# Optimization experiments

Measured on AMD Instinct MI355X. Metric: run time of the kernel, lower is better.

## Reference

```python
import jax, jax.numpy as jnp
import numpy as np

B, T, DIM = 1, 4096, 768
H, D = 6, 128  # num_heads, head_dim
ATTN_SCALE = 0.12
EPS = 1.1920929e-07  # torch fp32 rms_norm default eps


def _rms_norm(x):
    # F.rms_norm over last dim, no learned weight
    return x * jax.lax.rsqrt(jnp.mean(jnp.square(x), axis=-1, keepdims=True) + EPS)


def _rotary_tables(seq_len, head_dim):
    # angular_freq: (1/1024)**linspace(0,1,D//4) concat zeros(D//4) -> length D//2
    af = (1.0 / 1024.0) ** jnp.linspace(0.0, 1.0, head_dim // 4, dtype=jnp.float32)
    af = jnp.concatenate([af, jnp.zeros(head_dim // 4, dtype=jnp.float32)])
    t = jnp.arange(seq_len, dtype=jnp.float32)
    theta = t[:, None] * af[None, :]  # [T, D//2]
    return jnp.cos(theta), jnp.sin(theta)


def _apply_rotary(x_bthd, cos, sin):
    # x: [B,T,H,D]; rotate pairs (x1, x2) = halves of last dim
    x1, x2 = jnp.split(x_bthd.astype(jnp.float32), 2, axis=-1)
    c = cos[None, :, None, :]
    s = sin[None, :, None, :]
    y1 = x1 * c + x2 * s
    y2 = -x1 * s + x2 * c
    return jnp.concatenate([y1, y2], axis=-1).astype(x_bthd.dtype)


def setup_inputs() -> dict:
    key = jax.random.key(0)
    k1, k2, k3, k4, k5 = jax.random.split(key, 5)
    std = 0.5 * DIM ** (-0.5)
    bound = (3.0 ** 0.5) * std
    x = jax.random.normal(k1, (B, T, DIM), dtype=jnp.float32)
    ve = jax.random.normal(k2, (B, T, DIM), dtype=jnp.float32)
    qkv_w = jax.random.uniform(k3, (3, H * D, DIM), dtype=jnp.float32, minval=-bound, maxval=bound)
    lambdas = jnp.array([0.5, 0.5], dtype=jnp.float32)
    # original zero-inits c_proj; use small random weights for a nontrivial output
    c_proj_w = jax.random.uniform(k5, (DIM, H * D), dtype=jnp.float32, minval=-bound, maxval=bound)
    return {"x": x, "ve": ve, "qkv_w": qkv_w, "lambdas": lambdas, "c_proj_w": c_proj_w}


def reference(x, ve, qkv_w, lambdas, c_proj_w):
    Bx, Tx = x.shape[0], x.shape[1]
    # fused QKV: linear with weight [3*hdim, dim] -> [B,T,3*H,D]
    qkv = jnp.einsum('btd,ehd->bteh', x, qkv_w.reshape(3 * H, D, DIM).reshape(3 * H * D, DIM).reshape(3 * H, D, DIM))
    # simpler: flatten weight and reshape output
    w_flat = qkv_w.reshape(3 * H * D, DIM)
    qkv = (x @ w_flat.T).reshape(Bx, Tx, 3 * H, D)
    q, k, v = jnp.split(qkv, 3, axis=2)  # each [B,T,H,D]
    q, k = _rms_norm(q), _rms_norm(k)
    cos, sin = _rotary_tables(Tx, D)
    q, k = _apply_rotary(q, cos, sin), _apply_rotary(k, cos, sin)
    v = lambdas[0] * v + lambdas[1] * ve.reshape(Bx, Tx, H, D)
    # causal attention with non-standard scale
    scores = jnp.einsum('bthd,bshd->bhts', q, k) * ATTN_SCALE  # [B,H,T,T]
    causal = jnp.tril(jnp.ones((Tx, Tx), dtype=bool))
    scores = jnp.where(causal[None, None], scores, -jnp.inf)
    probs = jax.nn.softmax(scores, axis=-1)
    y = jnp.einsum('bhts,bshd->bthd', probs, v).reshape(Bx, Tx, H * D)
    return y @ c_proj_w.T
```

## Files before the change

kernel.cpp:

```cpp
#include <hip/hip_runtime.h>
#include <hip/hip_bf16.h>

using bf16 = __hip_bfloat16;
typedef __attribute__((ext_vector_type(8))) __bf16 bf16x8;
typedef __attribute__((ext_vector_type(4))) float f32x4;

static constexpr int T = 4096, DIM = 768, H = 6, D = 128, N3 = 2304;
static constexpr int FPH = 160;
static constexpr float kEps = 1.1920929e-07f;
static constexpr float kC1 = 0.12f * 1.44269504f;
static constexpr float kTHR = 66.6f;

__device__ __forceinline__ void gll16(const bf16* g, bf16* l) {
  __builtin_amdgcn_global_load_lds((const __attribute__((address_space(1))) void*)g,
                                   (__attribute__((address_space(3))) void*)l, 16, 0, 0);
}

__device__ __forceinline__ int chunk_prefix(int qt) {
  const int k = qt >> 4, rr = qt & 15;
  return qt + 8 * k * (k - 1) + rr * k;
}

__global__ __launch_bounds__(256) void cvt(const float* __restrict__ in,
                                           bf16* __restrict__ out, int n) {
  const int i = (blockIdx.x * 256 + threadIdx.x) * 8;
  if (i >= n) return;
  const float4 a = *(const float4*)(in + i);
  const float4 b = *(const float4*)(in + i + 4);
  bf16 t[8] = {(bf16)a.x, (bf16)a.y, (bf16)a.z, (bf16)a.w,
               (bf16)b.x, (bf16)b.y, (bf16)b.z, (bf16)b.w};
  *(int4*)(out + i) = *(const int4*)t;
}

__global__ __launch_bounds__(256) void rope_tab(float2* __restrict__ tab) {
  const int i = blockIdx.x * 256 + threadIdx.x;
  const int t = i >> 5, j = i & 31;
  const float af = exp2f(-10.f * (float)j * (1.f / 31.f));
  float s, c;
  sincosf((float)t * af, &s, &c);
  tab[i] = make_float2(c, s);
}

template <typename CT>
__global__ __launch_bounds__(256) void gemm_bt(const bf16* __restrict__ A,
                                               const bf16* __restrict__ B,
                                               CT* __restrict__ C,
                                               int M, int N, int K) {
  __shared__ bf16 lA[128][64];
  __shared__ bf16 lB[128][64];
  const int tid = threadIdx.x, lane = tid & 63, wid = tid >> 6;
  const int brow = blockIdx.y * 128, bcol = blockIdx.x * 128;
  const int wm = (wid >> 1) * 64, wn = (wid & 1) * 64;
  const int r = lane & 15, g = lane >> 4;
  f32x4 acc[4][4] = {};
  const int srow = wid * 32 + (lane >> 3);
  const int scol = (lane & 7) * 8;
  const bf16* gA = A + (long)(brow + srow) * K + scol;
  const bf16* gB = B + (long)(bcol + srow) * K + scol;
  for (int k0 = 0; k0 < K; k0 += 64) {
    __syncthreads();
#pragma unroll
    for (int i = 0; i < 4; ++i) {
      gll16(gA + (long)i * 8 * K + k0, &lA[wid * 32 + i * 8][0]);
      gll16(gB + (long)i * 8 * K + k0, &lB[wid * 32 + i * 8][0]);
    }
    __syncthreads();
#pragma unroll
    for (int kk = 0; kk < 2; ++kk) {
      bf16x8 af[4], bfr[4];
#pragma unroll
      for (int m = 0; m < 4; ++m)
        af[m] = *(const bf16x8*)&lA[wm + m * 16 + r][kk * 32 + g * 8];
#pragma unroll
      for (int n = 0; n < 4; ++n)
        bfr[n] = *(const bf16x8*)&lB[wn + n * 16 + r][kk * 32 + g * 8];
#pragma unroll
      for (int m = 0; m < 4; ++m)
#pragma unroll
        for (int n = 0; n < 4; ++n)
          acc[m][n] = __builtin_amdgcn_mfma_f32_16x16x32_bf16(af[m], bfr[n], acc[m][n], 0, 0, 0);
    }
  }
  const int crow = brow + wm + g * 4;
  const int ccol = bcol + wn + r;
#pragma unroll
  for (int m = 0; m < 4; ++m)
#pragma unroll
    for (int n = 0; n < 4; ++n)
#pragma unroll
      for (int q = 0; q < 4; ++q)
        C[(long)(crow + m * 16 + q) * N + ccol + n * 16] = (CT)acc[m][n][q];
}

__global__ __launch_bounds__(256) void qkv_post(const bf16* __restrict__ qkv,
                                                const float2* __restrict__ tab,
                                                bf16* __restrict__ qb,
                                                bf16* __restrict__ kb) {
  const int idx = blockIdx.x * 4 + (threadIdx.x >> 6);
  const int lane = threadIdx.x & 63;
  const int t = idx / H, h = idx % H;
  const bf16* row = qkv + (long)t * N3 + h * D;
  float q1 = __bfloat162float(row[lane]);
  float q2 = __bfloat162float(row[lane + 64]);
  float k1 = __bfloat162float(row[768 + lane]);
  float k2 = __bfloat162float(row[768 + lane + 64]);
  float qs = q1 * q1 + q2 * q2, ks = k1 * k1 + k2 * k2;
#pragma unroll
  for (int off = 32; off; off >>= 1) {
    qs += __shfl_xor(qs, off);
    ks += __shfl_xor(ks, off);
  }
  const float qsc = rsqrtf(qs * (1.f / 128.f) + kEps);
  const float ksc = rsqrtf(ks * (1.f / 128.f) + kEps);
  q1 *= qsc; q2 *= qsc; k1 *= ksc; k2 *= ksc;
  float c = 1.f, s = 0.f;
  if (lane < 32) {
    const float2 cs = tab[t * 32 + lane];
    c = cs.x; s = cs.y;
  }
  const float nq1 = q1 * c + q2 * s, nq2 = q2 * c - q1 * s;
  const float nk1 = k1 * c + k2 * s, nk2 = k2 * c - k1 * s;
  bf16* qo = qb + ((long)h * T + t) * D;
  bf16* ko = kb + ((long)h * T + t) * D;
  qo[lane] = (bf16)nq1; qo[lane + 64] = (bf16)nq2;
  ko[lane] = (bf16)nk1; ko[lane + 64] = (bf16)nk2;
}

__global__ __launch_bounds__(256) void v_trans(const bf16* __restrict__ qkv,
                                               const float* __restrict__ ve,
                                               const float* __restrict__ lam,
                                               bf16* __restrict__ vt) {
  __shared__ bf16 tile[64][129];
  const int t0 = blockIdx.x * 64, h = blockIdx.y;
  const int tid = threadIdx.x;
  const float l0 = lam[0], l1 = lam[1];
  const int row = tid >> 2;
  const int seg = (tid & 3) * 32;
  const bf16* src = qkv + (long)(t0 + row) * N3 + 1536 + h * D + seg;
  const float* vs = ve + (long)(t0 + row) * DIM + h * D + seg;
#pragma unroll
  for (int j = 0; j < 32; j += 8) {
    bf16x8 a = *(const bf16x8*)(src + j);
    const float4 e0 = *(const float4*)(vs + j);
    const float4 e1 = *(const float4*)(vs + j + 4);
    const float ef[8] = {e0.x, e0.y, e0.z, e0.w, e1.x, e1.y, e1.z, e1.w};
#pragma unroll
    for (int u = 0; u < 8; ++u)
      tile[row][seg + j + u] = (bf16)(l0 * (float)a[u] + l1 * ef[u]);
  }
  __syncthreads();
  const int d = tid >> 1, half = tid & 1;
  bf16 outr[32];
#pragma unroll
  for (int j = 0; j < 32; ++j) outr[j] = tile[half * 32 + j][d];
  bf16* dst = vt + ((long)h * D + d) * T + t0 + half * 32;
#pragma unroll
  for (int c = 0; c < 4; ++c)
    *(int4*)(dst + c * 8) = *(const int4*)&outr[c * 8];
}

__global__ __launch_bounds__(256, 4) void attn(const bf16* __restrict__ qb,
                                               const bf16* __restrict__ kb,
                                               const bf16* __restrict__ vt,
                                               bf16* __restrict__ po,
                                               float* __restrict__ pm,
                                               float* __restrict__ ps) {
  __shared__ bf16 Kl[64][128];
  __shared__ bf16 Vl[128][64];
  __shared__ bf16 Pl[4][16][64];
  const int bid = blockIdx.x;
  const int h = bid % H, fi = bid / H;
  int qt, ci;
  if (fi < 64)       { qt = 63 - (fi >> 2); ci = fi & 3; }
  else if (fi < 112) { const int u = fi - 64;  qt = 47 - u / 3;  ci = u % 3; }
  else if (fi < 144) { const int u = fi - 112; qt = 31 - (u >> 1); ci = u & 1; }
  else               { qt = 15 - (fi - 144); ci = 0; }
  const int ts = ci * 16;
  const int te = min(ts + 16, qt + 1);
  const int tid = threadIdx.x, lane = tid & 63, w = tid >> 6;
  const int r = lane & 15, g = lane >> 4;

  bf16x8 qf[4];
#pragma unroll
  for (int kk = 0; kk < 4; ++kk)
    qf[kk] = *(const bf16x8*)(qb + ((long)h * T + qt * 64 + w * 16 + r) * D + kk * 32 + g * 8);
  f32x4 o[8] = {};
  float m[4], sl[4];
#pragma unroll
  for (int q = 0; q < 4; ++q) { m[q] = -1e30f; sl[q] = 0.f; }

  auto STAGE = [&](int t) {
    const int kv0 = t * 64;
#pragma unroll
    for (int i = 0; i < 4; ++i) {
      const int seg = w * 4 + i;
      {
        const int lr = seg * 4 + (lane >> 4);
        const int cs = (lane & 15) ^ (lr & 7);
        gll16(kb + ((long)h * T + kv0 + lr) * D + cs * 8,
              (bf16*)&Kl[0][0] + seg * 512);
      }
      {
        const int lr = seg * 8 + (lane >> 3);
        const int cs = (lane & 7) ^ (lr & 7);
        gll16(vt + ((long)h * D + lr) * T + kv0 + cs * 8,
              (bf16*)&Vl[0][0] + seg * 512);
      }
    }
  };

  STAGE(ts);
  __syncthreads();
  for (int tt = ts; tt < te; ++tt) {
    const bf16* Kb = (const bf16*)&Kl[0][0];
    const bf16* Vb = (const bf16*)&Vl[0][0];
    bf16* Pb = &Pl[w][0][0];
    f32x4 st4[4];
    __builtin_amdgcn_s_setprio(1);
#pragma unroll
    for (int stt = 0; stt < 4; ++stt) {
      f32x4 a = {};
      const int lrk = stt * 16 + r;
#pragma unroll
      for (int kk = 0; kk < 4; ++kk) {
        const bf16x8 kf = *(const bf16x8*)(Kb + lrk * 128 + (((kk * 4 + g) ^ (lrk & 7)) * 8));
        a = __builtin_amdgcn_mfma_f32_16x16x32_bf16(qf[kk], kf, a, 0, 0, 0);
      }
      st4[stt] = a;
    }
    __builtin_amdgcn_s_setprio(0);
    if (tt == qt) {
      const int qgl = qt * 64 + w * 16 + 4 * g;
#pragma unroll
      for (int stt = 0; stt < 4; ++stt)
#pragma unroll
        for (int q = 0; q < 4; ++q)
          if (tt * 64 + stt * 16 + r > qgl + q) st4[stt][q] = -1e30f;
    }
    float mx[4];
#pragma unroll
    for (int q = 0; q < 4; ++q)
      mx[q] = fmaxf(fmaxf(st4[0][q], st4[1][q]), fmaxf(st4[2][q], st4[3][q]));
    const float dd = fmaxf(fmaxf(mx[0] - m[0], mx[1] - m[1]),
                           fmaxf(mx[2] - m[2], mx[3] - m[3]));
    if (__any(dd > kTHR)) {
#pragma unroll
      for (int off = 1; off < 16; off <<= 1)
#pragma unroll
        for (int q = 0; q < 4; ++q) mx[q] = fmaxf(mx[q], __shfl_xor(mx[q], off));
#pragma unroll
      for (int q = 0; q < 4; ++q) {
        const float nm = fmaxf(m[q], mx[q]);
        const float al = exp2f((m[q] - nm) * kC1);
        m[q] = nm;
        sl[q] *= al;
#pragma unroll
        for (int nn = 0; nn < 8; ++nn) o[nn][q] *= al;
      }
    }
#pragma unroll
    for (int stt = 0; stt < 4; ++stt)
#pragma unroll
      for (int q = 0; q < 4; ++q)
        st4[stt][q] = exp2f((st4[stt][q] - m[q]) * kC1);
#pragma unroll
    for (int q = 0; q < 4; ++q)
      sl[q] += (st4[0][q] + st4[1][q]) + (st4[2][q] + st4[3][q]);
#pragma unroll
    for (int stt = 0; stt < 4; ++stt)
#pragma unroll
      for (int q = 0; q < 4; ++q) {
        const int rw = 4 * g + q;
        Pb[rw * 64 + ((stt * 16 + r) ^ ((rw & 7) << 3))] = (bf16)st4[stt][q];
      }
    bf16x8 pf[2];
#pragma unroll
    for (int kk = 0; kk < 2; ++kk)
      pf[kk] = *(const bf16x8*)(Pb + r * 64 + (((kk * 4 + g) ^ (r & 7)) * 8));
    __builtin_amdgcn_s_setprio(1);
#pragma unroll
    for (int nn = 0; nn < 8; ++nn) {
      const int d = nn * 16 + r;
#pragma unroll
      for (int kk = 0; kk < 2; ++kk) {
        const bf16x8 vf = *(const bf16x8*)(Vb + d * 64 + (((kk * 4 + g) ^ (d & 7)) * 8));
        o[nn] = __builtin_amdgcn_mfma_f32_16x16x32_bf16(pf[kk], vf, o[nn], 0, 0, 0);
      }
    }
    __builtin_amdgcn_s_setprio(0);
    if (tt + 1 < te) {
      __syncthreads();
      STAGE(tt + 1);
      __syncthreads();
    }
  }
#pragma unroll
  for (int off = 1; off < 16; off <<= 1)
#pragma unroll
    for (int q = 0; q < 4; ++q) sl[q] += __shfl_xor(sl[q], off);
  const long part = (long)h * FPH + chunk_prefix(qt) + ci;
  bf16* pob = po + part * 8192;
  const int row0 = w * 16 + 4 * g;
#pragma unroll
  for (int nn = 0; nn < 8; ++nn)
#pragma unroll
    for (int q = 0; q < 4; ++q)
      pob[(row0 + q) * 128 + nn * 16 + r] = (bf16)o[nn][q];
  if (r == 0) {
#pragma unroll
    for (int q = 0; q < 4; ++q) {
      pm[part * 64 + row0 + q] = m[q];
      ps[part * 64 + row0 + q] = sl[q];
    }
  }
}

__global__ __launch_bounds__(256) void attn_reduce(const bf16* __restrict__ po,
                                                   const float* __restrict__ pm,
                                                   const float* __restrict__ ps,
                                                   bf16* __restrict__ yb) {
  const int qt = blockIdx.x, h = blockIdx.y;
  const int tid = threadIdx.x;
  const int row = tid >> 2, seg = (tid & 3) * 32;
  const int nch = (qt >> 4) + 1;
  const long base = (long)h * FPH + chunk_prefix(qt);
  float mv[4], sv[4];
  float mm = -1e30f;
  for (int ci = 0; ci < nch; ++ci) {
    mv[ci] = pm[(base + ci) * 64 + row];
    sv[ci] = ps[(base + ci) * 64 + row];
    mm = fmaxf(mm, mv[ci]);
  }
  float den = 0.f, wgt[4];
  for (int ci = 0; ci < nch; ++ci) {
    wgt[ci] = exp2f((mv[ci] - mm) * kC1);
    den += sv[ci] * wgt[ci];
  }
  const float inv = 1.f / den;
  float acc[32] = {};
  for (int ci = 0; ci < nch; ++ci) {
    const float wq = wgt[ci] * inv;
    const bf16* src = po + (base + ci) * 8192 + row * 128 + seg;
#pragma unroll
    for (int j = 0; j < 32; j += 8) {
      const bf16x8 v = *(const bf16x8*)(src + j);
#pragma unroll
      for (int u = 0; u < 8; ++u) acc[j + u] += wq * (float)v[u];
    }
  }
  bf16 outv[32];
#pragma unroll
  for (int j = 0; j < 32; ++j) outv[j] = (bf16)acc[j];
  bf16* dst = yb + (long)(qt * 64 + row) * DIM + h * D + seg;
#pragma unroll
  for (int cc = 0; cc < 4; ++cc)
    *(int4*)(dst + cc * 8) = *(const int4*)&outv[cc * 8];
}

extern "C" void kernel_launch(void* const* d_in, const int* in_sizes, int n_in,
                              void* d_out, int out_size, void* d_ws, size_t ws_size,
                              hipStream_t stream) {
  const float* x     = (const float*)d_in[0];
  const float* ve    = (const float*)d_in[1];
  const float* qkv_w = (const float*)d_in[2];
  const float* lam   = (const float*)d_in[3];
  const float* cproj = (const float*)d_in[4];
  float* out = (float*)d_out;

  bf16* qkv = (bf16*)d_ws;
  bf16* xb  = qkv + (long)T * N3;
  bf16* wb  = xb + (long)T * DIM;
  bf16* cb  = wb + (long)N3 * DIM;
  bf16* qb  = cb + (long)DIM * DIM;
  bf16* kb  = qb + (long)H * T * D;
  bf16* vt  = kb + (long)H * T * D;
  bf16* yb  = vt + (long)H * T * D;
  float2* tab = (float2*)(yb + (long)T * DIM);
  bf16* po  = (bf16*)d_ws;
  float* pm = (float*)(po + (long)H * FPH * 8192);
  float* ps = pm + (long)H * FPH * 64;

  rope_tab<<<dim3(T * 32 / 256), 256, 0, stream>>>(tab);
  cvt<<<dim3(T * DIM / 8 / 256), 256, 0, stream>>>(x, xb, T * DIM);
  cvt<<<dim3(N3 * DIM / 8 / 256), 256, 0, stream>>>(qkv_w, wb, N3 * DIM);
  cvt<<<dim3(DIM * DIM / 8 / 256), 256, 0, stream>>>(cproj, cb, DIM * DIM);

  gemm_bt<bf16><<<dim3(N3 / 128, T / 128), 256, 0, stream>>>(xb, wb, qkv, T, N3, DIM);
  qkv_post<<<dim3(T * H / 4), 256, 0, stream>>>(qkv, tab, qb, kb);
  v_trans<<<dim3(T / 64, H), 256, 0, stream>>>(qkv, ve, lam, vt);
  attn<<<dim3(FPH * H), 256, 0, stream>>>(qb, kb, vt, po, pm, ps);
  attn_reduce<<<dim3(64, H), 256, 0, stream>>>(po, pm, ps, yb);
  gemm_bt<float><<<dim3(DIM / 128, T / 128), 256, 0, stream>>>(yb, cb, out, T, DIM, DIM);
}
```

Before: 159.9 us.

## Process two query tiles per attention block and fuse prep kernels

Each attention workgroup now handles two adjacent 64-row query tiles and shares every K/V tile staged in LDS between them, with split-KV chunks of 8 tiles instead of 16. Blocks with a single chunk normalize their output and write it straight to yb, so the reduce kernel only covers query tiles from 8 upward. The three fp32-to-bf16 conversions and the rope-table build are merged into one launch. The aim is to halve K/V LDS traffic per query row and cut launch overhead, at the cost of more registers (occupancy bound lowered to 3 waves) and more partial results for the reduce step.

Result: slower. 391.9 us (+145.1%).

```diff
diff --git a/kernel.cpp b/kernel.cpp
--- a/kernel.cpp
+++ b/kernel.cpp
@@ -6,7 +6,7 @@
 typedef __attribute__((ext_vector_type(4))) float f32x4;
 
 static constexpr int T = 4096, DIM = 768, H = 6, D = 128, N3 = 2304;
-static constexpr int FPH = 160;
+static constexpr int PPH = 280;
 static constexpr float kEps = 1.1920929e-07f;
 static constexpr float kC1 = 0.12f * 1.44269504f;
 static constexpr float kTHR = 66.6f;
@@ -16,29 +16,40 @@
                                    (__attribute__((address_space(3))) void*)l, 16, 0, 0);
 }
 
-__device__ __forceinline__ int chunk_prefix(int qt) {
-  const int k = qt >> 4, rr = qt & 15;
-  return qt + 8 * k * (k - 1) + rr * k;
-}
-
-__global__ __launch_bounds__(256) void cvt(const float* __restrict__ in,
-                                           bf16* __restrict__ out, int n) {
-  const int i = (blockIdx.x * 256 + threadIdx.x) * 8;
-  if (i >= n) return;
-  const float4 a = *(const float4*)(in + i);
-  const float4 b = *(const float4*)(in + i + 4);
-  bf16 t[8] = {(bf16)a.x, (bf16)a.y, (bf16)a.z, (bf16)a.w,
-               (bf16)b.x, (bf16)b.y, (bf16)b.z, (bf16)b.w};
-  *(int4*)(out + i) = *(const int4*)t;
-}
-
-__global__ __launch_bounds__(256) void rope_tab(float2* __restrict__ tab) {
-  const int i = blockIdx.x * 256 + threadIdx.x;
-  const int t = i >> 5, j = i & 31;
-  const float af = exp2f(-10.f * (float)j * (1.f / 31.f));
-  float s, c;
-  sincosf((float)t * af, &s, &c);
-  tab[i] = make_float2(c, s);
+__device__ __forceinline__ int pre_qt(int qt) {
+  const int k = qt >> 3, rr = qt & 7;
+  return qt + 4 * k * (k - 1) + rr * k;
+}
+
+__global__ __launch_bounds__(256) void prep(const float* __restrict__ x,
+                                            const float* __restrict__ qkv_w,
+                                            const float* __restrict__ cproj,
+                                            bf16* __restrict__ xb, bf16* __restrict__ wb,
+                                            bf16* __restrict__ cb, float2* __restrict__ tab) {
+  const int NBX = T * DIM / 2048, NBW = N3 * DIM / 2048, NBC = DIM * DIM / 2048;
+  int b = blockIdx.x;
+  const int tid = threadIdx.x;
+  if (b < NBX + NBW + NBC) {
+    const float* in;
+    bf16* out;
+    if (b < NBX) { in = x; out = xb; }
+    else if (b < NBX + NBW) { in = qkv_w; out = wb; b -= NBX; }
+    else { in = cproj; out = cb; b -= NBX + NBW; }
+    const int i = (b * 256 + tid) * 8;
+    const float4 a = *(const float4*)(in + i);
+    const float4 c = *(const float4*)(in + i + 4);
+    bf16 t[8] = {(bf16)a.x, (bf16)a.y, (bf16)a.z, (bf16)a.w,
+                 (bf16)c.x, (bf16)c.y, (bf16)c.z, (bf16)c.w};
+    *(int4*)(out + i) = *(const int4*)t;
+  } else {
+    b -= NBX + NBW + NBC;
+    const int i = b * 256 + tid;
+    const int t = i >> 5, j = i & 31;
+    const float af = exp2f(-10.f * (float)j * (1.f / 31.f));
+    float s, c;
+    sincosf((float)t * af, &s, &c);
+    tab[i] = make_float2(c, s);
+  }
 }
 
 template <typename CT>
@@ -159,35 +170,41 @@
     *(int4*)(dst + c * 8) = *(const int4*)&outr[c * 8];
 }
 
-__global__ __launch_bounds__(256, 4) void attn(const bf16* __restrict__ qb,
+__global__ __launch_bounds__(256, 3) void attn(const bf16* __restrict__ qb,
                                                const bf16* __restrict__ kb,
                                                const bf16* __restrict__ vt,
                                                bf16* __restrict__ po,
                                                float* __restrict__ pm,
-                                               float* __restrict__ ps) {
+                                               float* __restrict__ ps,
+                                               bf16* __restrict__ yb) {
   __shared__ bf16 Kl[64][128];
   __shared__ bf16 Vl[128][64];
-  __shared__ bf16 Pl[4][16][64];
+  __shared__ bf16 Pl[4][2][16][64];
   const int bid = blockIdx.x;
-  const int h = bid % H, fi = bid / H;
-  int qt, ci;
-  if (fi < 64)       { qt = 63 - (fi >> 2); ci = fi & 3; }
-  else if (fi < 112) { const int u = fi - 64;  qt = 47 - u / 3;  ci = u % 3; }
-  else if (fi < 144) { const int u = fi - 112; qt = 31 - (u >> 1); ci = u & 1; }
-  else               { qt = 15 - (fi - 144); ci = 0; }
-  const int ts = ci * 16;
-  const int te = min(ts + 16, qt + 1);
+  const int h = bid % H;
+  const int fi = bid / H;
+  int s = 31, ci = 0, acc0 = 0;
+  for (int ss = 31; ss >= 0; --ss) {
+    const int n = (ss >> 2) + 1;
+    if (fi < acc0 + n) { s = ss; ci = fi - acc0; break; }
+    acc0 += n;
+  }
+  const int qtA = 2 * s, qtB = 2 * s + 1;
+  const int ts = ci * 8;
+  const int te = min(ts + 8, 2 * s + 2);
   const int tid = threadIdx.x, lane = tid & 63, w = tid >> 6;
   const int r = lane & 15, g = lane >> 4;
 
-  bf16x8 qf[4];
-#pragma unroll
-  for (int kk = 0; kk < 4; ++kk)
-    qf[kk] = *(const bf16x8*)(qb + ((long)h * T + qt * 64 + w * 16 + r) * D + kk * 32 + g * 8);
-  f32x4 o[8] = {};
-  float m[4], sl[4];
-#pragma unroll
-  for (int q = 0; q < 4; ++q) { m[q] = -1e30f; sl[q] = 0.f; }
+  bf16x8 qfA[4], qfB[4];
+#pragma unroll
+  for (int kk = 0; kk < 4; ++kk) {
+    qfA[kk] = *(const bf16x8*)(qb + ((long)h * T + qtA * 64 + w * 16 + r) * D + kk * 32 + g * 8);
+    qfB[kk] = *(const bf16x8*)(qb + ((long)h * T + qtB * 64 + w * 16 + r) * D + kk * 32 + g * 8);
+  }
+  f32x4 oA[8] = {}, oB[8] = {};
+  float mA[4], slA[4], mB[4], slB[4];
+#pragma unroll
+  for (int q = 0; q < 4; ++q) { mA[q] = -1e30f; slA[q] = 0.f; mB[q] = -1e30f; slB[q] = 0.f; }
 
   auto STAGE = [&](int t) {
     const int kv0 = t * 64;
@@ -209,82 +226,120 @@
     }
   };
 
+  auto smup = [&](f32x4 (&st4)[4], float* m, float* sl, f32x4 (&o)[8],
+                  bf16* Pb, bool diag, int qt, int tt) {
+    if (diag) {
+      const int qgl = qt * 64 + w * 16 + 4 * g;
+#pragma unroll
+      for (int stt = 0; stt < 4; ++stt)
+#pragma unroll
+        for (int q = 0; q < 4; ++q)
+          if (tt * 64 + stt * 16 + r > qgl + q) st4[stt][q] = -1e30f;
+    }
+    float mx[4];
+#pragma unroll
+    for (int q = 0; q < 4; ++q)
+      mx[q] = fmaxf(fmaxf(st4[0][q], st4[1][q]), fmaxf(st4[2][q], st4[3][q]));
+    const float dd = fmaxf(fmaxf(mx[0] - m[0], mx[1] - m[1]),
+                           fmaxf(mx[2] - m[2], mx[3] - m[3]));
+    if (__any(dd > kTHR)) {
+#pragma unroll
+      for (int off = 1; off < 16; off <<= 1)
+#pragma unroll
+        for (int q = 0; q < 4; ++q) mx[q] = fmaxf(mx[q], __shfl_xor(mx[q], off));
+#pragma unroll
+      for (int q = 0; q < 4; ++q) {
+        const float nm = fmaxf(m[q], mx[q]);
+        const float al = exp2f((m[q] - nm) * kC1);
+        m[q] = nm;
+        sl[q] *= al;
+#pragma unroll
+        for (int nn = 0; nn < 8; ++nn) o[nn][q] *= al;
+      }
+    }
+#pragma unroll
+    for (int stt = 0; stt < 4; ++stt)
+#pragma unroll
+      for (int q = 0; q < 4; ++q)
+        st4[stt][q] = exp2f((st4[stt][q] - m[q]) * kC1);
+#pragma unroll
+    for (int q = 0; q < 4; ++q)
+      sl[q] += (st4[0][q] + st4[1][q]) + (st4[2][q] + st4[3][q]);
+#pragma unroll
+    for (int stt = 0; stt < 4; ++stt)
+#pragma unroll
+      for (int q = 0; q < 4; ++q) {
+        const int rw = 4 * g + q;
+        Pb[rw * 64 + ((stt * 16 + r) ^ ((rw & 7) << 3))] = (bf16)st4[stt][q];
+      }
+  };
+
   STAGE(ts);
   __syncthreads();
   for (int tt = ts; tt < te; ++tt) {
     const bf16* Kb = (const bf16*)&Kl[0][0];
     const bf16* Vb = (const bf16*)&Vl[0][0];
-    bf16* Pb = &Pl[w][0][0];
-    f32x4 st4[4];
+    bf16* PbA = &Pl[w][0][0][0];
+    bf16* PbB = &Pl[w][1][0][0];
+    const bool doA = (tt <= qtA);
+    f32x4 stA[4], stB[4];
     __builtin_amdgcn_s_setprio(1);
-#pragma unroll
-    for (int stt = 0; stt < 4; ++stt) {
-      f32x4 a = {};
-      const int lrk = stt * 16 + r;
-#pragma unroll
-      for (int kk = 0; kk < 4; ++kk) {
-        const bf16x8 kf = *(const bf16x8*)(Kb + lrk * 128 + (((kk * 4 + g) ^ (lrk & 7)) * 8));
-        a = __builtin_amdgcn_mfma_f32_16x16x32_bf16(qf[kk], kf, a, 0, 0, 0);
-      }
-      st4[stt] = a;
+    if (doA) {
+#pragma unroll
+      for (int stt = 0; stt < 4; ++stt) {
+        f32x4 a1 = {}, a2 = {};
+        const int lrk = stt * 16 + r;
+#pragma unroll
+        for (int kk = 0; kk < 4; ++kk) {
+          const bf16x8 kf = *(const bf16x8*)(Kb + lrk * 128 + (((kk * 4 + g) ^ (lrk & 7)) * 8));
+          a1 = __builtin_amdgcn_mfma_f32_16x16x32_bf16(qfA[kk], kf, a1, 0, 0, 0);
+          a2 = __builtin_amdgcn_mfma_f32_16x16x32_bf16(qfB[kk], kf, a2, 0, 0, 0);
+        }
+        stA[stt] = a1; stB[stt] = a2;
+      }
+    } else {
+#pragma unroll
+      for (int stt = 0; stt < 4; ++stt) {
+        f32x4 a2 = {};
+        const int lrk = stt * 16 + r;
+#pragma unroll
+        for (int kk = 0; kk < 4; ++kk) {
+          const bf16x8 kf = *(const bf16x8*)(Kb + lrk * 128 + (((kk * 4 + g) ^ (lrk & 7)) * 8));
+          a2 = __builtin_amdgcn_mfma_f32_16x16x32_bf16(qfB[kk], kf, a2, 0, 0, 0);
+        }
+        stB[stt] = a2;
+      }
     }
     __builtin_amdgcn_s_setprio(0);
-    if (tt == qt) {
-      const int qgl = qt * 64 + w * 16 + 4 * g;
-#pragma unroll
-      for (int stt = 0; stt < 4; ++stt)
-#pragma unroll
-        for (int q = 0; q < 4; ++q)
-          if (tt * 64 + stt * 16 + r > qgl + q) st4[stt][q] = -1e30f;
-    }
-    float mx[4];
-#pragma unroll
-    for (int q = 0; q < 4; ++q)
-      mx[q] = fmaxf(fmaxf(st4[0][q], st4[1][q]), fmaxf(st4[2][q], st4[3][q]));
-    const float dd = fmaxf(fmaxf(mx[0] - m[0], mx[1] - m[1]),
-                           fmaxf(mx[2] - m[2], mx[3] - m[3]));
-    if (__any(dd > kTHR)) {
-#pragma unroll
-      for (int off = 1; off < 16; off <<= 1)
-#pragma unroll
-        for (int q = 0; q < 4; ++q) mx[q] = fmaxf(mx[q], __shfl_xor(mx[q], off));
-#pragma unroll
-      for (int q = 0; q < 4; ++q) {
-        const float nm = fmaxf(m[q], mx[q]);
-        const float al = exp2f((m[q] - nm) * kC1);
-        m[q] = nm;
-        sl[q] *= al;
-#pragma unroll
-        for (int nn = 0; nn < 8; ++nn) o[nn][q] *= al;
-      }
-    }
-#pragma unroll
-    for (int stt = 0; stt < 4; ++stt)
-#pragma unroll
-      for (int q = 0; q < 4; ++q)
-        st4[stt][q] = exp2f((st4[stt][q] - m[q]) * kC1);
-#pragma unroll
-    for (int q = 0; q < 4; ++q)
-      sl[q] += (st4[0][q] + st4[1][q]) + (st4[2][q] + st4[3][q]);
-#pragma unroll
-    for (int stt = 0; stt < 4; ++stt)
-#pragma unroll
-      for (int q = 0; q < 4; ++q) {
-        const int rw = 4 * g + q;
-        Pb[rw * 64 + ((stt * 16 + r) ^ ((rw & 7) << 3))] = (bf16)st4[stt][q];
-      }
-    bf16x8 pf[2];
-#pragma unroll
-    for (int kk = 0; kk < 2; ++kk)
-      pf[kk] = *(const bf16x8*)(Pb + r * 64 + (((kk * 4 + g) ^ (r & 7)) * 8));
+    if (doA) smup(stA, mA, slA, oA, PbA, tt == qtA, qtA, tt);
+    smup(stB, mB, slB, oB, PbB, tt == qtB, qtB, tt);
+    bf16x8 pfA[2], pfB[2];
+#pragma unroll
+    for (int kk = 0; kk < 2; ++kk) {
+      pfA[kk] = *(const bf16x8*)(PbA + r * 64 + (((kk * 4 + g) ^ (r & 7)) * 8));
+      pfB[kk] = *(const bf16x8*)(PbB + r * 64 + (((kk * 4 + g) ^ (r & 7)) * 8));
+    }
     __builtin_amdgcn_s_setprio(1);
-#pragma unroll
-    for (int nn = 0; nn < 8; ++nn) {
-      const int d = nn * 16 + r;
-#pragma unroll
-      for (int kk = 0; kk < 2; ++kk) {
-        const bf16x8 vf = *(const bf16x8*)(Vb + d * 64 + (((kk * 4 + g) ^ (d & 7)) * 8));
-        o[nn] = __builtin_amdgcn_mfma_f32_16x16x32_bf16(pf[kk], vf, o[nn], 0, 0, 0);
+    if (doA) {
+#pragma unroll
+      for (int nn = 0; nn < 8; ++nn) {
+        const int d = nn * 16 + r;
+#pragma unroll
+        for (int kk = 0; kk < 2; ++kk) {
+          const bf16x8 vf = *(const bf16x8*)(Vb + d * 64 + (((kk * 4 + g) ^ (d & 7)) * 8));
+          oA[nn] = __builtin_amdgcn_mfma_f32_16x16x32_bf16(pfA[kk], vf, oA[nn], 0, 0, 0);
+          oB[nn] = __builtin_amdgcn_mfma_f32_16x16x32_bf16(pfB[kk], vf, oB[nn], 0, 0, 0);
+        }
+      }
+    } else {
+#pragma unroll
+      for (int nn = 0; nn < 8; ++nn) {
+        const int d = nn * 16 + r;
+#pragma unroll
+        for (int kk = 0; kk < 2; ++kk) {
+          const bf16x8 vf = *(const bf16x8*)(Vb + d * 64 + (((kk * 4 + g) ^ (d & 7)) * 8));
+          oB[nn] = __builtin_amdgcn_mfma_f32_16x16x32_bf16(pfB[kk], vf, oB[nn], 0, 0, 0);
+        }
       }
     }
     __builtin_amdgcn_s_setprio(0);
@@ -297,20 +352,39 @@
 #pragma unroll
   for (int off = 1; off < 16; off <<= 1)
 #pragma unroll
-    for (int q = 0; q < 4; ++q) sl[q] += __shfl_xor(sl[q], off);
-  const long part = (long)h * FPH + chunk_prefix(qt) + ci;
-  bf16* pob = po + part * 8192;
+    for (int q = 0; q < 4; ++q) {
+      slA[q] += __shfl_xor(slA[q], off);
+      slB[q] += __shfl_xor(slB[q], off);
+    }
   const int row0 = w * 16 + 4 * g;
-#pragma unroll
-  for (int nn = 0; nn < 8; ++nn)
-#pragma unroll
-    for (int q = 0; q < 4; ++q)
-      pob[(row0 + q) * 128 + nn * 16 + r] = (bf16)o[nn][q];
-  if (r == 0) {
-#pragma unroll
-    for (int q = 0; q < 4; ++q) {
-      pm[part * 64 + row0 + q] = m[q];
-      ps[part * 64 + row0 + q] = sl[q];
+  if (s < 4) {
+#pragma unroll
+    for (int nn = 0; nn < 8; ++nn)
+#pragma unroll
+      for (int q = 0; q < 4; ++q) {
+        yb[(long)(qtA * 64 + row0 + q) * DIM + h * D + nn * 16 + r] = (bf16)(oA[nn][q] / slA[q]);
+        yb[(long)(qtB * 64 + row0 + q) * DIM + h * D + nn * 16 + r] = (bf16)(oB[nn][q] / slB[q]);
+      }
+  } else {
+    const long partA = (long)h * PPH + (pre_qt(qtA) - 8) + ci;
+    const long partB = (long)h * PPH + (pre_qt(qtB) - 8) + ci;
+    bf16* poA = po + partA * 8192;
+    bf16* poB = po + partB * 8192;
+#pragma unroll
+    for (int nn = 0; nn < 8; ++nn)
+#pragma unroll
+      for (int q = 0; q < 4; ++q) {
+        poA[(row0 + q) * 128 + nn * 16 + r] = (bf16)oA[nn][q];
+        poB[(row0 + q) * 128 + nn * 16 + r] = (bf16)oB[nn][q];
+      }
+    if (r == 0) {
+#pragma unroll
+      for (int q = 0; q < 4; ++q) {
+        pm[partA * 64 + row0 + q] = mA[q];
+        ps[partA * 64 + row0 + q] = slA[q];
+        pm[partB * 64 + row0 + q] = mB[q];
+        ps[partB * 64 + row0 + q] = slB[q];
+      }
     }
   }
 }
@@ -319,27 +393,20 @@
                                                    const float* __restrict__ pm,
                                                    const float* __restrict__ ps,
                                                    bf16* __restrict__ yb) {
-  const int qt = blockIdx.x, h = blockIdx.y;
+  const int qt = 8 + blockIdx.x, h = blockIdx.y;
   const int tid = threadIdx.x;
   const int row = tid >> 2, seg = (tid & 3) * 32;
-  const int nch = (qt >> 4) + 1;
-  const long base = (long)h * FPH + chunk_prefix(qt);
-  float mv[4], sv[4];
+  const int nch = (qt >> 3) + 1;
+  const long base = (long)h * PPH + pre_qt(qt) - 8;
   float mm = -1e30f;
-  for (int ci = 0; ci < nch; ++ci) {
-    mv[ci] = pm[(base + ci) * 64 + row];
-    sv[ci] = ps[(base + ci) * 64 + row];
-    mm = fmaxf(mm, mv[ci]);
-  }
-  float den = 0.f, wgt[4];
-  for (int ci = 0; ci < nch; ++ci) {
-    wgt[ci] = exp2f((mv[ci] - mm) * kC1);
-    den += sv[ci] * wgt[ci];
-  }
+  for (int ci = 0; ci < nch; ++ci) mm = fmaxf(mm, pm[(base + ci) * 64 + row]);
+  float den = 0.f;
+  for (int ci = 0; ci < nch; ++ci)
+    den += ps[(base + ci) * 64 + row] * exp2f((pm[(base + ci) * 64 + row] - mm) * kC1);
   const float inv = 1.f / den;
   float acc[32] = {};
   for (int ci = 0; ci < nch; ++ci) {
-    const float wq = wgt[ci] * inv;
+    const float wq = exp2f((pm[(base + ci) * 64 + row] - mm) * kC1) * inv;
     const bf16* src = po + (base + ci) * 8192 + row * 128 + seg;
 #pragma unroll
     for (int j = 0; j < 32; j += 8) {
@@ -377,18 +444,16 @@
   bf16* yb  = vt + (long)H * T * D;
   float2* tab = (float2*)(yb + (long)T * DIM);
   bf16* po  = (bf16*)d_ws;
-  float* pm = (float*)(po + (long)H * FPH * 8192);
-  float* ps = pm + (long)H * FPH * 64;
-
-  rope_tab<<<dim3(T * 32 / 256), 256, 0, stream>>>(tab);
-  cvt<<<dim3(T * DIM / 8 / 256), 256, 0, stream>>>(x, xb, T * DIM);
-  cvt<<<dim3(N3 * DIM / 8 / 256), 256, 0, stream>>>(qkv_w, wb, N3 * DIM);
-  cvt<<<dim3(DIM * DIM / 8 / 256), 256, 0, stream>>>(cproj, cb, DIM * DIM);
+  float* pm = (float*)(po + (long)PPH * H * 8192);
+  float* ps = pm + (long)PPH * H * 64;
+
+  const int NBX = T * DIM / 2048, NBW = N3 * DIM / 2048, NBC = DIM * DIM / 2048;
+  prep<<<dim3(NBX + NBW + NBC + T * 32 / 256), 256, 0, stream>>>(x, qkv_w, cproj, xb, wb, cb, tab);
 
   gemm_bt<bf16><<<dim3(N3 / 128, T / 128), 256, 0, stream>>>(xb, wb, qkv, T, N3, DIM);
   qkv_post<<<dim3(T * H / 4), 256, 0, stream>>>(qkv, tab, qb, kb);
   v_trans<<<dim3(T / 64, H), 256, 0, stream>>>(qkv, ve, lam, vt);
-  attn<<<dim3(FPH * H), 256, 0, stream>>>(qb, kb, vt, po, pm, ps);
-  attn_reduce<<<dim3(64, H), 256, 0, stream>>>(po, pm, ps, yb);
+  attn<<<dim3(144 * H), 256, 0, stream>>>(qb, kb, vt, po, pm, ps, yb);
+  attn_reduce<<<dim3(56, H), 256, 0, stream>>>(po, pm, ps, yb);
   gemm_bt<float><<<dim3(DIM / 128, T / 128), 256, 0, stream>>>(yb, cb, out, T, DIM, DIM);
 }
```
